# Performance work log

Hardware: AMD Instinct MI355X
Metric: run time of the kernel (lower is better)

Reference implementation:

```python
import jax, jax.numpy as jnp
import numpy as np

EPS = 1e-5  # torch LayerNorm default
H = 8       # num_heads


def _ln(x, w, b):
    mu = jnp.mean(x, axis=-1, keepdims=True)
    var = jnp.mean(jnp.square(x - mu), axis=-1, keepdims=True)
    return (x - mu) * jax.lax.rsqrt(var + EPS) * w + b


def setup_inputs() -> dict:
    key = jax.random.key(0)
    ks = jax.random.split(key, 8)
    B, N, C = 4, 2048, 512
    d_ff = 4 * C
    g = lambda k, shape: jax.random.normal(k, shape, jnp.float32) * 0.02
    return {
        "x": jax.random.normal(ks[0], (B, N, C), jnp.float32),
        "e": jax.random.normal(ks[1], (B, N, C), jnp.float32),
        "w_qkv": g(ks[2], (C, 3 * C)),
        "w_s": g(ks[3], (C, C)),
        "w_gate": g(ks[4], (C, C)),
        "w_proj": g(ks[5], (C, C)),
        "b_proj": jnp.zeros((C,), jnp.float32),
        "ln1_w": jnp.ones((C,), jnp.float32), "ln1_b": jnp.zeros((C,), jnp.float32),
        "ln2_w": jnp.ones((C,), jnp.float32), "ln2_b": jnp.zeros((C,), jnp.float32),
        "ln3_w": jnp.ones((C,), jnp.float32), "ln3_b": jnp.zeros((C,), jnp.float32),
        "w_fc1": g(ks[6], (C, d_ff)), "b_fc1": jnp.zeros((d_ff,), jnp.float32),
        "w_fc2": g(ks[7], (d_ff, C)), "b_fc2": jnp.zeros((C,), jnp.float32),
    }


def reference(x, e, w_qkv, w_s, w_gate, w_proj, b_proj,
              ln1_w, ln1_b, ln2_w, ln2_b, ln3_w, ln3_b,
              w_fc1, b_fc1, w_fc2, b_fc2):
    B, N, C = x.shape
    D = C // H
    scale = D ** -0.5  # qk_scale=None -> (dim//num_heads)**-0.5

    # --- attention branch: x + attn(norm1(x), norm2(e)) ---
    xn = _ln(x, ln1_w, ln1_b)
    en = _ln(e, ln2_w, ln2_b)
    qkv = (xn @ w_qkv).reshape(B, N, 3, H, D).transpose(2, 0, 3, 1, 4)  # [3,B,H,N,D]
    q, k, v = qkv[0], qkv[1], qkv[2]
    s = (en @ w_s).reshape(B, N, H, D).transpose(0, 2, 1, 3)            # [B,H,N,D]
    attn = jax.nn.softmax(jnp.einsum('bhnd,bhmd->bhnm', q, k + s) * scale, axis=-1)
    o = jnp.einsum('bhnm,bhmd->bhnd', attn, v).transpose(0, 2, 1, 3).reshape(B, N, C)
    o = (o * (xn @ w_gate)) @ w_proj + b_proj
    x = x + o  # drop_path is identity (drop_prob=0)

    # --- MLP branch: x + mlp(norm3(x)) ---
    xn3 = _ln(x, ln3_w, ln3_b)
    h = jax.nn.gelu(xn3 @ w_fc1 + b_fc1, approximate=False)  # torch nn.GELU = exact erf
    return x + (h @ w_fc2 + b_fc2)
```

## Files before the change

### kernel.cpp

```cpp
#include <hip/hip_runtime.h>

typedef unsigned short u16;
typedef short s16;
typedef u16 u16x4 __attribute__((ext_vector_type(4)));
typedef u16 u16x8 __attribute__((ext_vector_type(8)));
typedef s16 s16x8 __attribute__((ext_vector_type(8)));
typedef float f32x4 __attribute__((ext_vector_type(4)));

__device__ __forceinline__ float b2f(u16 u) {
  union { unsigned int i; float f; } v;
  v.i = ((unsigned int)u) << 16;
  return v.f;
}
__device__ __forceinline__ u16 f2b(float f) {
  union { float f; unsigned int i; } v;
  v.f = f;
  unsigned int r = v.i + 0x7fffu + ((v.i >> 16) & 1u);
  return (u16)(r >> 16);
}
__device__ __forceinline__ u16 f2bt(float f) {
  union { float f; unsigned int i; } v;
  v.f = f;
  return (u16)(v.i >> 16);
}
__device__ __forceinline__ unsigned packtrunc(float hi, float lo) {
  union { float f; unsigned int i; } a, b;
  a.f = hi; b.f = lo;
  return __builtin_amdgcn_perm(a.i, b.i, 0x07060302u);
}

#define MFMA16(a, b, c) __builtin_amdgcn_mfma_f32_16x16x32_bf16(a, b, c, 0, 0, 0)

__device__ __forceinline__ void gld16(const u16* g, u16* l) {
  __builtin_amdgcn_global_load_lds(
      (const __attribute__((address_space(1))) void*)g,
      (__attribute__((address_space(3))) void*)l, 16, 0, 0);
}

__global__ __launch_bounds__(256) void prep_kernel(
    const float* __restrict__ wq, const float* __restrict__ wsc,
    const float* __restrict__ wg, const float* __restrict__ wp,
    const float* __restrict__ w1, const float* __restrict__ w2,
    u16* __restrict__ wqgT, u16* __restrict__ wsT, u16* __restrict__ wpT,
    u16* __restrict__ wf1T, u16* __restrict__ wf2T,
    const float* __restrict__ x, const float* __restrict__ e,
    const float* __restrict__ ln1w, const float* __restrict__ ln1b,
    const float* __restrict__ ln2w, const float* __restrict__ ln2b,
    u16* __restrict__ xn, u16* __restrict__ en) {
  __shared__ float T[64][65];
  int bid = blockIdx.x;
  if (bid < 896) {
    const float* src; u16* dst; int K, N, ntiles;
    if (bid < 192)      { src = wq;  dst = wqgT;              K = 512;  N = 1536; ntiles = 24; }
    else if (bid < 256) { src = wg;  dst = wqgT + 1536 * 512; K = 512;  N = 512;  ntiles = 8; bid -= 192; }
    else if (bid < 320) { src = wsc; dst = wsT;               K = 512;  N = 512;  ntiles = 8; bid -= 256; }
    else if (bid < 384) { src = wp;  dst = wpT;               K = 512;  N = 512;  ntiles = 8; bid -= 320; }
    else if (bid < 640) { src = w1;  dst = wf1T;              K = 512;  N = 2048; ntiles = 32; bid -= 384; }
    else                { src = w2;  dst = wf2T;              K = 2048; N = 512;  ntiles = 8; bid -= 640; }
    const int n0 = (bid % ntiles) * 64, k0 = (bid / ntiles) * 64;
    const int c = threadIdx.x & 63, r0 = threadIdx.x >> 6;
#pragma unroll
    for (int i = 0; i < 16; i++) {
      const int r = i * 4 + r0;
      T[r][c] = src[(size_t)(k0 + r) * N + n0 + c];
    }
    __syncthreads();
#pragma unroll
    for (int i = 0; i < 16; i++) {
      const int r = i * 4 + r0;
      dst[(size_t)(n0 + r) * K + k0 + c] = f2b(T[c][r]);
    }
    return;
  }
  bid -= 896;
  const float *inv, *w, *bb;
  u16* out;
  if (bid < 2048) { inv = x; w = ln1w; bb = ln1b; out = xn; }
  else { bid -= 2048; inv = e; w = ln2w; bb = ln2b; out = en; }
  const int row = bid * 4 + (threadIdx.x >> 6);
  const int lane = threadIdx.x & 63;
  const float* p = inv + (size_t)row * 512 + lane * 8;
  f32x4 v0 = *(const f32x4*)p;
  f32x4 v1 = *(const f32x4*)(p + 4);
  float xv[8];
#pragma unroll
  for (int i = 0; i < 4; i++) { xv[i] = v0[i]; xv[4 + i] = v1[i]; }
  float s = 0.f;
#pragma unroll
  for (int i = 0; i < 8; i++) s += xv[i];
#pragma unroll
  for (int m = 1; m < 64; m <<= 1) s += __shfl_xor(s, m, 64);
  const float mu = s * (1.0f / 512.0f);
  float vs = 0.f;
#pragma unroll
  for (int i = 0; i < 8; i++) { const float d = xv[i] - mu; vs += d * d; }
#pragma unroll
  for (int m = 1; m < 64; m <<= 1) vs += __shfl_xor(vs, m, 64);
  const float r = rsqrtf(vs * (1.0f / 512.0f) + 1e-5f);
  const f32x4 w0 = *(const f32x4*)(w + lane * 8);
  const f32x4 w1v = *(const f32x4*)(w + lane * 8 + 4);
  const f32x4 bb0 = *(const f32x4*)(bb + lane * 8);
  const f32x4 bb1 = *(const f32x4*)(bb + lane * 8 + 4);
  u16x8 ov;
#pragma unroll
  for (int i = 0; i < 4; i++) {
    ov[i] = f2b((xv[i] - mu) * r * w0[i] + bb0[i]);
    ov[4 + i] = f2b((xv[4 + i] - mu) * r * w1v[i] + bb1[i]);
  }
  *(u16x8*)(out + (size_t)row * 512 + lane * 8) = ov;
}

__global__ __launch_bounds__(256) void ln_kernel(const float* __restrict__ inv,
                                                 const float* __restrict__ w,
                                                 const float* __restrict__ bvec,
                                                 u16* __restrict__ out) {
  const int row = blockIdx.x * 4 + (threadIdx.x >> 6);
  const int lane = threadIdx.x & 63;
  const float* p = inv + (size_t)row * 512 + lane * 8;
  f32x4 v0 = *(const f32x4*)p;
  f32x4 v1 = *(const f32x4*)(p + 4);
  float x[8];
#pragma unroll
  for (int i = 0; i < 4; i++) { x[i] = v0[i]; x[4 + i] = v1[i]; }
  float s = 0.f;
#pragma unroll
  for (int i = 0; i < 8; i++) s += x[i];
#pragma unroll
  for (int m = 1; m < 64; m <<= 1) s += __shfl_xor(s, m, 64);
  const float mu = s * (1.0f / 512.0f);
  float vs = 0.f;
#pragma unroll
  for (int i = 0; i < 8; i++) { const float d = x[i] - mu; vs += d * d; }
#pragma unroll
  for (int m = 1; m < 64; m <<= 1) vs += __shfl_xor(vs, m, 64);
  const float r = rsqrtf(vs * (1.0f / 512.0f) + 1e-5f);
  const f32x4 w0 = *(const f32x4*)(w + lane * 8);
  const f32x4 w1 = *(const f32x4*)(w + lane * 8 + 4);
  const f32x4 b0 = *(const f32x4*)(bvec + lane * 8);
  const f32x4 b1 = *(const f32x4*)(bvec + lane * 8 + 4);
  u16x8 ov;
#pragma unroll
  for (int i = 0; i < 4; i++) {
    ov[i] = f2b((x[i] - mu) * r * w0[i] + b0[i]);
    ov[4 + i] = f2b((x[4 + i] - mu) * r * w1[i] + b1[i]);
  }
  *(u16x8*)(out + (size_t)row * 512 + lane * 8) = ov;
}

enum { EPI_NONE = 0, EPI_F32RES = 1, EPI_GELU = 2 };

template<int EPI, int BM, int BK>
__global__ __launch_bounds__(256) void mgemm(const u16* __restrict__ A,
                                             const u16* __restrict__ Bt,
                                             int M, int N, int K,
                                             u16* __restrict__ Cb, float* Cf,
                                             const float* __restrict__ bias,
                                             const float* resf) {
  constexpr int NT = (BM == 128) ? 4 : 2;
  constexpr int ACHW = BM * BK / 512 / 4;
  constexpr int BCHW = 128 * BK / 512 / 4;
  constexpr int LPR = BK / 8;
  constexpr int RPC = 512 / BK;
  __shared__ u16 As[BM * BK];
  __shared__ u16 Bs[128 * BK];
  const int tid = threadIdx.x;
  const int wv = tid >> 6, lane = tid & 63;
  const int quad = lane >> 4, l16 = lane & 15;
  const int sw = l16 & 7;
  const int wrow = (BM == 128) ? (wv >> 1) * 64 : 0;
  const int wcol = (BM == 128) ? (wv & 1) * 64 : wv * 32;
  const int m0 = blockIdx.y * BM, n0 = blockIdx.x * 128;
  const int lrow = lane / LPR;
  const int inrow = lane % LPR;
  f32x4 acc[4][NT];
#pragma unroll
  for (int i = 0; i < 4; i++)
#pragma unroll
    for (int j = 0; j < NT; j++) acc[i][j] = (f32x4){0.f, 0.f, 0.f, 0.f};
  for (int k0 = 0; k0 < K; k0 += BK) {
    __syncthreads();
#pragma unroll
    for (int i = 0; i < ACHW; i++) {
      const int ch = wv * ACHW + i;
      const int r = ch * RPC + lrow;
      gld16(A + (size_t)(m0 + r) * K + k0 + ((inrow ^ (r & 7)) * 8), &As[ch * 512]);
    }
#pragma unroll
    for (int i = 0; i < BCHW; i++) {
      const int ch = wv * BCHW + i;
      const int r = ch * RPC + lrow;
      gld16(Bt + (size_t)(n0 + r) * K + k0 + ((inrow ^ (r & 7)) * 8), &Bs[ch * 512]);
    }
    __syncthreads();
#pragma unroll
    for (int ks = 0; ks < BK / 32; ks++) {
      s16x8 af[4], bf[NT];
#pragma unroll
      for (int mt = 0; mt < 4; mt++)
        af[mt] = *(const s16x8*)&As[(wrow + mt * 16 + l16) * BK +
                                    (((ks * 4 + quad) ^ sw) * 8)];
#pragma unroll
      for (int nt = 0; nt < NT; nt++)
        bf[nt] = *(const s16x8*)&Bs[(wcol + nt * 16 + l16) * BK +
                                    (((ks * 4 + quad) ^ sw) * 8)];
#pragma unroll
      for (int mt = 0; mt < 4; mt++)
#pragma unroll
        for (int nt = 0; nt < NT; nt++)
          acc[mt][nt] = MFMA16(af[mt], bf[nt], acc[mt][nt]);
    }
  }
#pragma unroll
  for (int nt = 0; nt < NT; nt++) {
    const int n = n0 + wcol + nt * 16 + l16;
    const float bn = (EPI != EPI_NONE) ? bias[n] : 0.f;
#pragma unroll
    for (int mt = 0; mt < 4; mt++) {
#pragma unroll
      for (int r = 0; r < 4; r++) {
        const int m = m0 + wrow + mt * 16 + quad * 4 + r;
        float v = acc[mt][nt][r] + bn;
        if (EPI == EPI_GELU)
          v = 0.5f * v * (1.0f + erff(v * 0.70710678118654752f));
        if (EPI == EPI_F32RES) {
          const size_t idx = (size_t)m * N + n;
          Cf[idx] = v + resf[idx];
        } else {
          Cb[(size_t)m * N + n] = f2bt(v);
        }
      }
    }
  }
}

__global__ __launch_bounds__(256) void sgvt_kernel(const u16* __restrict__ en,
                                                   const u16* __restrict__ wsT,
                                                   const u16* __restrict__ qg,
                                                   u16* __restrict__ ksg,
                                                   u16* __restrict__ vtg) {
  __shared__ u16 sh[24576];
  const int gid = blockIdx.x;
  const int tid = threadIdx.x;
  if (gid < 512) {
    u16* As = sh;
    u16* Bs = sh + 64 * 128;
    const int wv = tid >> 6, lane = tid & 63;
    const int quad = lane >> 4, l16 = lane & 15;
    const int sw = l16 & 7;
    const int wcol = wv * 32;
    const int m0 = (gid >> 2) * 64, n0 = (gid & 3) * 128;
    const int lrow = lane >> 4, inrow = lane & 15;
    f32x4 acc[4][2];
#pragma unroll
    for (int i = 0; i < 4; i++)
#pragma unroll
      for (int j = 0; j < 2; j++) acc[i][j] = (f32x4){0.f, 0.f, 0.f, 0.f};
    for (int k0 = 0; k0 < 512; k0 += 128) {
      __syncthreads();
#pragma unroll
      for (int i = 0; i < 4; i++) {
        const int ch = wv * 4 + i;
        const int r = ch * 4 + lrow;
        gld16(en + (size_t)(m0 + r) * 512 + k0 + ((inrow ^ (r & 7)) * 8), &As[ch * 512]);
      }
#pragma unroll
      for (int i = 0; i < 8; i++) {
        const int ch = wv * 8 + i;
        const int r = ch * 4 + lrow;
        gld16(wsT + (size_t)(n0 + r) * 512 + k0 + ((inrow ^ (r & 7)) * 8), &Bs[ch * 512]);
      }
      __syncthreads();
#pragma unroll
      for (int ks = 0; ks < 4; ks++) {
        s16x8 af[4], bf[2];
#pragma unroll
        for (int mt = 0; mt < 4; mt++)
          af[mt] = *(const s16x8*)&As[(mt * 16 + l16) * 128 + (((ks * 4 + quad) ^ sw) * 8)];
#pragma unroll
        for (int nt = 0; nt < 2; nt++)
          bf[nt] = *(const s16x8*)&Bs[(wcol + nt * 16 + l16) * 128 + (((ks * 4 + quad) ^ sw) * 8)];
#pragma unroll
        for (int mt = 0; mt < 4; mt++)
#pragma unroll
          for (int nt = 0; nt < 2; nt++)
            acc[mt][nt] = MFMA16(af[mt], bf[nt], acc[mt][nt]);
      }
    }
#pragma unroll
    for (int nt = 0; nt < 2; nt++) {
      const int n = n0 + wcol + nt * 16 + l16;
#pragma unroll
      for (int mt = 0; mt < 4; mt++) {
#pragma unroll
        for (int r = 0; r < 4; r++) {
          const int m = m0 + mt * 16 + quad * 4 + r;
          float v = acc[mt][nt][r] + b2f(qg[(size_t)m * 2048 + 512 + n]);
          const int b = m >> 11, kk = m & 2047, h = n >> 6, d = n & 63;
          ksg[(size_t)(b * 8 + h) * 131072 + (size_t)kk * 64 + d] = f2bt(v);
        }
      }
    }
  } else {
    u16* T = sh;
    const int vtid = gid - 512;
    const int bh = vtid >> 5;
    const int b = bh >> 3, h = bh & 7;
    const int kk0 = (vtid & 31) * 64;
    const size_t rb = (size_t)b * 2048;
    const size_t base = (size_t)bh * 131072;
    const int row = tid >> 2, cb = (tid & 3) * 16;
    const u16* vp = qg + (rb + kk0 + row) * 2048 + 1024 + h * 64 + cb;
    const u16x8 v0v = *(const u16x8*)vp;
    const u16x8 v1v = *(const u16x8*)(vp + 8);
    *(u16x8*)&T[row * 72 + cb] = v0v;
    *(u16x8*)&T[row * 72 + cb + 8] = v1v;
    __syncthreads();
    u16x8 a0, a1;
#pragma unroll
    for (int i = 0; i < 8; i++) {
      a0[i] = T[(cb + i) * 72 + row];
      a1[i] = T[(cb + 8 + i) * 72 + row];
    }
    *(u16x8*)(vtg + base + (size_t)row * 2048 + kk0 + cb) = a0;
    *(u16x8*)(vtg + base + (size_t)row * 2048 + kk0 + cb + 8) = a1;
  }
}

__global__ __launch_bounds__(256) void attn_kernel(const u16* __restrict__ qg,
                                                   const u16* __restrict__ ksg,
                                                   const u16* __restrict__ vtg,
                                                   u16* __restrict__ og) {
  __shared__ u16 KSs[64 * 64];
  __shared__ u16 VTs[64 * 64];
  __shared__ u16 PS[4][16 * 72];
  const int tid = threadIdx.x;
  const int w = tid >> 6, lane = tid & 63;
  const int quad = lane >> 4, l16 = lane & 15;
  const int sw = l16 & 7;
  const int q0 = blockIdx.x * 64;
  const int bh = blockIdx.y;
  const int h = bh & 7;
  const size_t rb = (size_t)(bh >> 3) * 2048;
  const size_t base = (size_t)bh * 131072;
  const int lrow = lane >> 3;
  const int lcs = ((lane & 7) ^ lrow) * 8;

  s16x8 aq[2];
  {
    const u16* qp = qg + (rb + q0 + w * 16 + l16) * 2048 + h * 64 + quad * 8;
#pragma unroll
    for (int ks = 0; ks < 2; ks++) {
      const u16x8 qv = *(const u16x8*)(qp + ks * 32);
      s16x8 t;
#pragma unroll
      for (int i = 0; i < 8; i++) t[i] = (s16)f2b(b2f(qv[i]) * 0.125f);
      aq[ks] = t;
    }
  }
  float l_run = 0.f;
  f32x4 oacc[4];
#pragma unroll
  for (int nt = 0; nt < 4; nt++) oacc[nt] = (f32x4){0.f, 0.f, 0.f, 0.f};

  for (int kt = 0; kt < 32; kt++) {
    const int kk0 = kt * 64;
    __syncthreads();
#pragma unroll
    for (int i = 0; i < 2; i++) {
      const int ch = w * 2 + i;
      gld16(ksg + base + (size_t)(kk0 + ch * 8 + lrow) * 64 + lcs, &KSs[ch * 512]);
      gld16(vtg + base + (size_t)(ch * 8 + lrow) * 2048 + kk0 + lcs, &VTs[ch * 512]);
    }
    __syncthreads();
    f32x4 sacc[4];
#pragma unroll
    for (int mt = 0; mt < 4; mt++) sacc[mt] = (f32x4){0.f, 0.f, 0.f, 0.f};
#pragma unroll
    for (int ks = 0; ks < 2; ks++) {
#pragma unroll
      for (int mt = 0; mt < 4; mt++) {
        const s16x8 kf = *(const s16x8*)&KSs[(mt * 16 + l16) * 64 +
                                             (((ks * 4 + quad) ^ sw) * 8)];
        sacc[mt] = MFMA16(kf, aq[ks], sacc[mt]);
      }
    }
#pragma unroll
    for (int mt = 0; mt < 4; mt++) {
      const float p0 = __expf(sacc[mt][0]);
      const float p1 = __expf(sacc[mt][1]);
      const float p2 = __expf(sacc[mt][2]);
      const float p3 = __expf(sacc[mt][3]);
      l_run += (p0 + p1) + (p2 + p3);
      uint2 pk;
      pk.x = packtrunc(p1, p0);
      pk.y = packtrunc(p3, p2);
      *(uint2*)&PS[w][l16 * 72 + mt * 16 + quad * 4] = pk;
    }
#pragma unroll
    for (int ks = 0; ks < 2; ks++) {
      const s16x8 pf = *(const s16x8*)&PS[w][l16 * 72 + ks * 32 + quad * 8];
#pragma unroll
      for (int nt = 0; nt < 4; nt++) {
        const s16x8 vf = *(const s16x8*)&VTs[(nt * 16 + l16) * 64 +
                                             (((ks * 4 + quad) ^ sw) * 8)];
        oacc[nt] = MFMA16(pf, vf, oacc[nt]);
      }
    }
  }
  l_run += __shfl_xor(l_run, 16, 64);
  l_run += __shfl_xor(l_run, 32, 64);
#pragma unroll
  for (int r = 0; r < 4; r++) {
    const float linv = 1.001953125f / __shfl(l_run, quad * 4 + r, 64);
    const size_t qrow = rb + q0 + w * 16 + quad * 4 + r;
    const size_t grow = qrow * 2048 + 1536 + h * 64;
    const size_t rowb = qrow * 512 + h * 64;
#pragma unroll
    for (int nt = 0; nt < 4; nt++) {
      const float gv = b2f(qg[grow + nt * 16 + l16]);
      og[rowb + nt * 16 + l16] = f2bt(oacc[nt][r] * linv * gv);
    }
  }
}

extern "C" void kernel_launch(void* const* d_in, const int* in_sizes, int n_in,
                              void* d_out, int out_size, void* d_ws, size_t ws_size,
                              hipStream_t stream) {
  const float* x      = (const float*)d_in[0];
  const float* e      = (const float*)d_in[1];
  const float* w_qkv  = (const float*)d_in[2];
  const float* w_s    = (const float*)d_in[3];
  const float* w_gate = (const float*)d_in[4];
  const float* w_proj = (const float*)d_in[5];
  const float* b_proj = (const float*)d_in[6];
  const float* ln1w   = (const float*)d_in[7];
  const float* ln1b   = (const float*)d_in[8];
  const float* ln2w   = (const float*)d_in[9];
  const float* ln2b   = (const float*)d_in[10];
  const float* ln3w   = (const float*)d_in[11];
  const float* ln3b   = (const float*)d_in[12];
  const float* w_fc1  = (const float*)d_in[13];
  const float* b_fc1  = (const float*)d_in[14];
  const float* w_fc2  = (const float*)d_in[15];
  const float* b_fc2  = (const float*)d_in[16];
  float* out = (float*)d_out;
  char* ws = (char*)d_ws;

  u16* xn    = (u16*)(ws + 0);
  u16* en    = (u16*)(ws + 8388608);
  u16* qg    = (u16*)(ws + 16777216);
  u16* ksg   = (u16*)(ws + 50331648);
  u16* obuf  = (u16*)(ws + 58720256);
  u16* wqgT  = (u16*)(ws + 67108864);
  u16* wsT   = (u16*)(ws + 69206016);
  u16* wpT   = (u16*)(ws + 69730304);
  u16* wf1T  = (u16*)(ws + 70254592);
  u16* wf2T  = (u16*)(ws + 72351744);
  u16* vtg   = (u16*)(ws + 74448896);
  u16* hbuf  = qg;
  u16* xn3   = xn;

  dim3 blk(256);
  prep_kernel<<<4992, blk, 0, stream>>>(w_qkv, w_s, w_gate, w_proj, w_fc1, w_fc2,
                                        wqgT, wsT, wpT, wf1T, wf2T,
                                        x, e, ln1w, ln1b, ln2w, ln2b, xn, en);
  mgemm<EPI_NONE, 128, 64><<<dim3(16, 64), blk, 0, stream>>>(
      xn, wqgT, 8192, 2048, 512, qg, nullptr, nullptr, nullptr);
  sgvt_kernel<<<1536, blk, 0, stream>>>(en, wsT, qg, ksg, vtg);
  attn_kernel<<<dim3(32, 32), blk, 0, stream>>>(qg, ksg, vtg, obuf);
  mgemm<EPI_F32RES, 64, 128><<<dim3(4, 128), blk, 0, stream>>>(
      obuf, wpT, 8192, 512, 512, nullptr, out, b_proj, x);
  ln_kernel<<<2048, blk, 0, stream>>>(out, ln3w, ln3b, xn3);
  mgemm<EPI_GELU, 128, 64><<<dim3(16, 64), blk, 0, stream>>>(
      xn3, wf1T, 8192, 2048, 512, hbuf, nullptr, b_fc1, nullptr);
  mgemm<EPI_F32RES, 64, 128><<<dim3(4, 128), blk, 0, stream>>>(
      hbuf, wf2T, 8192, 512, 2048, nullptr, out, b_fc2, out);
  (void)in_sizes; (void)n_in; (void)out_size; (void)ws_size;
}
```

Measured before the change: 329.0 us.

## Switch GEMMs to 32x32x16 MFMA and fold log2e into the query scale

```diff
diff --git a/kernel.cpp b/kernel.cpp
--- a/kernel.cpp
+++ b/kernel.cpp
@@ -1,4 +1,5 @@
 #include <hip/hip_runtime.h>
+#include <cmath>
 
 typedef unsigned short u16;
 typedef short s16;
@@ -6,6 +7,7 @@
 typedef u16 u16x8 __attribute__((ext_vector_type(8)));
 typedef s16 s16x8 __attribute__((ext_vector_type(8)));
 typedef float f32x4 __attribute__((ext_vector_type(4)));
+typedef float f32x16 __attribute__((ext_vector_type(16)));
 
 __device__ __forceinline__ float b2f(u16 u) {
   union { unsigned int i; float f; } v;
@@ -30,6 +32,7 @@
 }
 
 #define MFMA16(a, b, c) __builtin_amdgcn_mfma_f32_16x16x32_bf16(a, b, c, 0, 0, 0)
+#define MFMA32(a, b, c) __builtin_amdgcn_mfma_f32_32x32x16_bf16(a, b, c, 0, 0, 0)
 
 __device__ __forceinline__ void gld16(const u16* g, u16* l) {
   __builtin_amdgcn_global_load_lds(
@@ -156,7 +159,8 @@
                                              u16* __restrict__ Cb, float* Cf,
                                              const float* __restrict__ bias,
                                              const float* resf) {
-  constexpr int NT = (BM == 128) ? 4 : 2;
+  constexpr int MT = 2;
+  constexpr int NT = (BM == 128) ? 2 : 1;
   constexpr int ACHW = BM * BK / 512 / 4;
   constexpr int BCHW = 128 * BK / 512 / 4;
   constexpr int LPR = BK / 8;
@@ -165,18 +169,20 @@
   __shared__ u16 Bs[128 * BK];
   const int tid = threadIdx.x;
   const int wv = tid >> 6, lane = tid & 63;
-  const int quad = lane >> 4, l16 = lane & 15;
-  const int sw = l16 & 7;
+  const int l32 = lane & 31, hl = lane >> 5;
+  const int sw7 = lane & 7;
   const int wrow = (BM == 128) ? (wv >> 1) * 64 : 0;
   const int wcol = (BM == 128) ? (wv & 1) * 64 : wv * 32;
   const int m0 = blockIdx.y * BM, n0 = blockIdx.x * 128;
   const int lrow = lane / LPR;
   const int inrow = lane % LPR;
-  f32x4 acc[4][NT];
-#pragma unroll
-  for (int i = 0; i < 4; i++)
-#pragma unroll
-    for (int j = 0; j < NT; j++) acc[i][j] = (f32x4){0.f, 0.f, 0.f, 0.f};
+  f32x16 acc[MT][NT];
+#pragma unroll
+  for (int i = 0; i < MT; i++)
+#pragma unroll
+    for (int j = 0; j < NT; j++)
+#pragma unroll
+      for (int r = 0; r < 16; r++) acc[i][j][r] = 0.f;
   for (int k0 = 0; k0 < K; k0 += BK) {
     __syncthreads();
 #pragma unroll
@@ -193,33 +199,33 @@
     }
     __syncthreads();
 #pragma unroll
-    for (int ks = 0; ks < BK / 32; ks++) {
-      s16x8 af[4], bf[NT];
-#pragma unroll
-      for (int mt = 0; mt < 4; mt++)
-        af[mt] = *(const s16x8*)&As[(wrow + mt * 16 + l16) * BK +
-                                    (((ks * 4 + quad) ^ sw) * 8)];
+    for (int ks = 0; ks < BK / 16; ks++) {
+      s16x8 af[MT], bf[NT];
+#pragma unroll
+      for (int mt = 0; mt < MT; mt++)
+        af[mt] = *(const s16x8*)&As[(wrow + mt * 32 + l32) * BK +
+                                    (((ks * 2 + hl) ^ sw7) * 8)];
 #pragma unroll
       for (int nt = 0; nt < NT; nt++)
-        bf[nt] = *(const s16x8*)&Bs[(wcol + nt * 16 + l16) * BK +
-                                    (((ks * 4 + quad) ^ sw) * 8)];
-#pragma unroll
-      for (int mt = 0; mt < 4; mt++)
+        bf[nt] = *(const s16x8*)&Bs[(wcol + nt * 32 + l32) * BK +
+                                    (((ks * 2 + hl) ^ sw7) * 8)];
+#pragma unroll
+      for (int mt = 0; mt < MT; mt++)
 #pragma unroll
         for (int nt = 0; nt < NT; nt++)
-          acc[mt][nt] = MFMA16(af[mt], bf[nt], acc[mt][nt]);
+          acc[mt][nt] = MFMA32(af[mt], bf[nt], acc[mt][nt]);
     }
   }
 #pragma unroll
   for (int nt = 0; nt < NT; nt++) {
-    const int n = n0 + wcol + nt * 16 + l16;
+    const int n = n0 + wcol + nt * 32 + l32;
     const float bn = (EPI != EPI_NONE) ? bias[n] : 0.f;
 #pragma unroll
-    for (int mt = 0; mt < 4; mt++) {
-#pragma unroll
-      for (int r = 0; r < 4; r++) {
-        const int m = m0 + wrow + mt * 16 + quad * 4 + r;
-        float v = acc[mt][nt][r] + bn;
+    for (int mt = 0; mt < MT; mt++) {
+#pragma unroll
+      for (int reg = 0; reg < 16; reg++) {
+        const int m = m0 + wrow + mt * 32 + (reg & 3) + 8 * (reg >> 2) + 4 * hl;
+        float v = acc[mt][nt][reg] + bn;
         if (EPI == EPI_GELU)
           v = 0.5f * v * (1.0f + erff(v * 0.70710678118654752f));
         if (EPI == EPI_F32RES) {
@@ -245,16 +251,16 @@
     u16* As = sh;
     u16* Bs = sh + 64 * 128;
     const int wv = tid >> 6, lane = tid & 63;
-    const int quad = lane >> 4, l16 = lane & 15;
-    const int sw = l16 & 7;
+    const int l32 = lane & 31, hl = lane >> 5;
+    const int sw7 = lane & 7;
     const int wcol = wv * 32;
     const int m0 = (gid >> 2) * 64, n0 = (gid & 3) * 128;
     const int lrow = lane >> 4, inrow = lane & 15;
-    f32x4 acc[4][2];
-#pragma unroll
-    for (int i = 0; i < 4; i++)
-#pragma unroll
-      for (int j = 0; j < 2; j++) acc[i][j] = (f32x4){0.f, 0.f, 0.f, 0.f};
+    f32x16 acc[2];
+#pragma unroll
+    for (int i = 0; i < 2; i++)
+#pragma unroll
+      for (int r = 0; r < 16; r++) acc[i][r] = 0.f;
     for (int k0 = 0; k0 < 512; k0 += 128) {
       __syncthreads();
 #pragma unroll
@@ -271,33 +277,26 @@
       }
       __syncthreads();
 #pragma unroll
-      for (int ks = 0; ks < 4; ks++) {
-        s16x8 af[4], bf[2];
-#pragma unroll
-        for (int mt = 0; mt < 4; mt++)
-          af[mt] = *(const s16x8*)&As[(mt * 16 + l16) * 128 + (((ks * 4 + quad) ^ sw) * 8)];
-#pragma unroll
-        for (int nt = 0; nt < 2; nt++)
-          bf[nt] = *(const s16x8*)&Bs[(wcol + nt * 16 + l16) * 128 + (((ks * 4 + quad) ^ sw) * 8)];
-#pragma unroll
-        for (int mt = 0; mt < 4; mt++)
-#pragma unroll
-          for (int nt = 0; nt < 2; nt++)
-            acc[mt][nt] = MFMA16(af[mt], bf[nt], acc[mt][nt]);
-      }
-    }
-#pragma unroll
-    for (int nt = 0; nt < 2; nt++) {
-      const int n = n0 + wcol + nt * 16 + l16;
-#pragma unroll
-      for (int mt = 0; mt < 4; mt++) {
-#pragma unroll
-        for (int r = 0; r < 4; r++) {
-          const int m = m0 + mt * 16 + quad * 4 + r;
-          float v = acc[mt][nt][r] + b2f(qg[(size_t)m * 2048 + 512 + n]);
-          const int b = m >> 11, kk = m & 2047, h = n >> 6, d = n & 63;
-          ksg[(size_t)(b * 8 + h) * 131072 + (size_t)kk * 64 + d] = f2bt(v);
-        }
+      for (int ks = 0; ks < 8; ks++) {
+        s16x8 af[2], bfr;
+#pragma unroll
+        for (int mt = 0; mt < 2; mt++)
+          af[mt] = *(const s16x8*)&As[(mt * 32 + l32) * 128 + (((ks * 2 + hl) ^ sw7) * 8)];
+        bfr = *(const s16x8*)&Bs[(wcol + l32) * 128 + (((ks * 2 + hl) ^ sw7) * 8)];
+#pragma unroll
+        for (int mt = 0; mt < 2; mt++)
+          acc[mt] = MFMA32(af[mt], bfr, acc[mt]);
+      }
+    }
+    const int n = n0 + wcol + l32;
+#pragma unroll
+    for (int mt = 0; mt < 2; mt++) {
+#pragma unroll
+      for (int reg = 0; reg < 16; reg++) {
+        const int m = m0 + mt * 32 + (reg & 3) + 8 * (reg >> 2) + 4 * hl;
+        float v = acc[mt][reg] + b2f(qg[(size_t)m * 2048 + 512 + n]);
+        const int b = m >> 11, kk = m & 2047, h = n >> 6, d = n & 63;
+        ksg[(size_t)(b * 8 + h) * 131072 + (size_t)kk * 64 + d] = f2bt(v);
       }
     }
   } else {
@@ -353,7 +352,7 @@
       const u16x8 qv = *(const u16x8*)(qp + ks * 32);
       s16x8 t;
 #pragma unroll
-      for (int i = 0; i < 8; i++) t[i] = (s16)f2b(b2f(qv[i]) * 0.125f);
+      for (int i = 0; i < 8; i++) t[i] = (s16)f2b(b2f(qv[i]) * 0.1803368801111437f);
       aq[ks] = t;
     }
   }
@@ -386,10 +385,10 @@
     }
 #pragma unroll
     for (int mt = 0; mt < 4; mt++) {
-      const float p0 = __expf(sacc[mt][0]);
-      const float p1 = __expf(sacc[mt][1]);
-      const float p2 = __expf(sacc[mt][2]);
-      const float p3 = __expf(sacc[mt][3]);
+      const float p0 = exp2f(sacc[mt][0]);
+      const float p1 = exp2f(sacc[mt][1]);
+      const float p2 = exp2f(sacc[mt][2]);
+      const float p3 = exp2f(sacc[mt][3]);
       l_run += (p0 + p1) + (p2 + p3);
       uint2 pk;
       pk.x = packtrunc(p1, p0);
```

New measurement: 329.0 us. Within noise of the previous version (+0.0%).
